# Kernel tuning notes

Hardware: AMD Instinct MI355X
Metric: run time of the kernel (lower is better)

Reference implementation:

```python
import jax, jax.numpy as jnp
import numpy as np

D_MODEL, D_K, D_V = 1024, 64, 128
NUM_HEAD = D_MODEL // D_V  # 8


def setup_inputs() -> dict:
    key = jax.random.key(0)
    ks = jax.random.split(key, 6)
    B, SQ, SKV = 4, 2048, 2048
    return {
        "encoder_output": jax.random.normal(ks[0], (B, SKV, D_MODEL), jnp.float32),
        "pre_output": jax.random.normal(ks[1], (B, SQ, D_MODEL), jnp.float32),
        "Wq": jax.random.normal(ks[2], (D_MODEL, D_K * NUM_HEAD), jnp.float32) * 0.02,
        "Wk": jax.random.normal(ks[3], (D_MODEL, D_K * NUM_HEAD), jnp.float32) * 0.02,
        "Wv": jax.random.normal(ks[4], (D_MODEL, D_MODEL), jnp.float32) * 0.02,
        "Wo": jax.random.normal(ks[5], (D_MODEL, D_MODEL), jnp.float32) * 0.02,
    }


def reference(encoder_output, pre_output, Wq, Wk, Wv, Wo):
    B, SQ, _ = pre_output.shape
    SKV = encoder_output.shape[1]
    # projections (Linear, bias=False)
    q = pre_output @ Wq          # [B, SQ, H*d_k]
    k = encoder_output @ Wk      # [B, SKV, H*d_k]
    v = encoder_output @ Wv      # [B, SKV, H*d_v] (= d_model)
    # per-head contiguous slices == reshape into head dim
    q = q.reshape(B, SQ, NUM_HEAD, D_K)
    k = k.reshape(B, SKV, NUM_HEAD, D_K)
    v = v.reshape(B, SKV, NUM_HEAD, D_V)
    scale = 1.0 / np.sqrt(D_K).astype(np.float32)
    scores = jnp.einsum("bqhd,bkhd->bhqk", q, k) * scale  # [B,H,SQ,SKV]
    attn = jax.nn.softmax(scores, axis=-1)
    out = jnp.einsum("bhqk,bkhd->bqhd", attn, v)           # [B,SQ,H,d_v]
    out = out.reshape(B, SQ, NUM_HEAD * D_V)               # concat heads
    return out @ Wo
```

## Files before the change

### kernel.cpp

```cpp
#include <hip/hip_runtime.h>
#include <math.h>

#define D_MODEL 1024
#define DK 64
#define DV 128
#define NH 8
#define BB 4
#define SQL 2048
#define SKV 2048

typedef __bf16 bf16x8 __attribute__((ext_vector_type(8)));
typedef float f32x4 __attribute__((ext_vector_type(4)));

#if __has_builtin(__builtin_amdgcn_exp2f)
#define EXP2(x) __builtin_amdgcn_exp2f(x)
#else
#define EXP2(x) exp2f(x)
#endif

#define MFMA16(a, b, c) __builtin_amdgcn_mfma_f32_16x16x32_bf16(a, b, c, 0, 0, 0)

__device__ __forceinline__ ushort f2bf(float f) {
  unsigned u = __float_as_uint(f);
  u += 0x7FFFu + ((u >> 16) & 1u);
  return (ushort)(u >> 16);
}
__device__ __forceinline__ unsigned pk2bf(float lo, float hi) {
  unsigned ul = __float_as_uint(lo);
  unsigned uh = __float_as_uint(hi);
  ul += 0x7FFFu + ((ul >> 16) & 1u);
  uh += 0x7FFFu + ((uh >> 16) & 1u);
  return __builtin_amdgcn_perm(uh, ul, 0x07060302u);
}

#define GLDS16(g, l)                                                       \
  __builtin_amdgcn_global_load_lds(                                        \
      (const __attribute__((address_space(1))) unsigned int*)(g),          \
      (__attribute__((address_space(3))) unsigned int*)(l), 16, 0, 0)

__global__ __launch_bounds__(256) void cvt2_kernel(
    const float* __restrict__ s0, const float* __restrict__ s1,
    ushort* __restrict__ d0, ushort* __restrict__ d1, int n4) {
  const float* src = blockIdx.z ? s1 : s0;
  ushort* dst = blockIdx.z ? d1 : d0;
  int i = blockIdx.x * 256 + threadIdx.x;
  if (i >= n4) return;
  float4 v = ((const float4*)src)[i];
  ushort4 o;
  o.x = f2bf(v.x); o.y = f2bf(v.y); o.z = f2bf(v.z); o.w = f2bf(v.w);
  ((ushort4*)dst)[i] = o;
}

__global__ __launch_bounds__(256) void cvt_t4_kernel(
    const float* __restrict__ W0, const float* __restrict__ W1,
    const float* __restrict__ W2, const float* __restrict__ W3,
    ushort* __restrict__ T0, ushort* __restrict__ T1, ushort* __restrict__ T2,
    ushort* __restrict__ T3) {
  __shared__ ushort T[32][34];
  const int z = blockIdx.z;
  const int C = (z < 2) ? 512 : 1024;
  const int c0 = blockIdx.y * 32;
  if (c0 >= C) return;
  const float* W = (z == 0) ? W0 : (z == 1) ? W1 : (z == 2) ? W2 : W3;
  ushort* Wt = (z == 0) ? T0 : (z == 1) ? T1 : (z == 2) ? T2 : T3;
  const int R = 1024;
  const int r0 = blockIdx.x * 32;
  const int tx = threadIdx.x, ty = threadIdx.y;
#pragma unroll
  for (int i = 0; i < 4; ++i) {
    const int rr = ty + i * 8;
    T[rr][tx] = f2bf(W[(size_t)(r0 + rr) * C + c0 + tx]);
  }
  __syncthreads();
#pragma unroll
  for (int i = 0; i < 4; ++i) {
    const int rr = ty + i * 8;
    Wt[(size_t)(c0 + rr) * R + r0 + tx] = T[tx][rr];
  }
}

__device__ __forceinline__ void gemm_core_acc(ushort* sh, const ushort* At,
                                              const ushort* Bt, int K,
                                              f32x4 (&acc)[4][4]) {
  const int t = threadIdx.x;
  const int w = t >> 6, lane = t & 63;
  const int wm = (w >> 1) * 64, wn = (w & 1) * 64;
  const int lr = lane & 15, quad = lane >> 4;

  const int r0 = t >> 2;
  const int lb = (t & 3) ^ ((r0 >> 1) & 3);
  const ushort* gA0 = At + (size_t)r0 * K + lb * 8;
  const ushort* gA1 = At + (size_t)(r0 + 64) * K + lb * 8;
  const ushort* gB0 = Bt + (size_t)r0 * K + lb * 8;
  const ushort* gB1 = Bt + (size_t)(r0 + 64) * K + lb * 8;

  const int sw = (quad ^ ((lr >> 1) & 3)) * 8;

#pragma unroll
  for (int i = 0; i < 4; ++i)
#pragma unroll
    for (int j = 0; j < 4; ++j) acc[i][j] = (f32x4){0.f, 0.f, 0.f, 0.f};

  auto stage = [&](int k0, int buf) {
    ushort* d = sh + buf * 8192 + t * 8;
    GLDS16(gA0 + k0, d);
    GLDS16(gA1 + k0, d + 2048);
    GLDS16(gB0 + k0, d + 4096);
    GLDS16(gB1 + k0, d + 6144);
  };

  const int NT = K >> 5;
  stage(0, 0);
  for (int ti = 0; ti < NT; ++ti) {
    const bool more = (ti + 1 < NT);
    if (more) {
      stage((ti + 1) * 32, (ti + 1) & 1);
      asm volatile("s_waitcnt vmcnt(4)" ::: "memory");
    } else {
      asm volatile("s_waitcnt vmcnt(0)" ::: "memory");
    }
    __builtin_amdgcn_s_barrier();
    __builtin_amdgcn_sched_barrier(0);
    const ushort(*A)[32] = (const ushort(*)[32])(sh + (ti & 1) * 8192);
    const ushort(*B)[32] = (const ushort(*)[32])(sh + (ti & 1) * 8192 + 4096);
    bf16x8 fa[4], fb[4];
#pragma unroll
    for (int i = 0; i < 4; ++i) fa[i] = *(const bf16x8*)&A[wm + i * 16 + lr][sw];
#pragma unroll
    for (int j = 0; j < 4; ++j) fb[j] = *(const bf16x8*)&B[wn + j * 16 + lr][sw];
#pragma unroll
    for (int i = 0; i < 4; ++i)
#pragma unroll
      for (int j = 0; j < 4; ++j) acc[i][j] = MFMA16(fa[i], fb[j], acc[i][j]);
    __builtin_amdgcn_sched_barrier(0);
    if (more) __builtin_amdgcn_s_barrier();
  }
}

__global__ __launch_bounds__(256) void gemm_qkv_kernel(
    const ushort* __restrict__ preb, const ushort* __restrict__ encb,
    const ushort* __restrict__ WqkvT, ushort* __restrict__ qb,
    ushort* __restrict__ kb, ushort* __restrict__ vt, float qsc) {
  __shared__ __attribute__((aligned(16))) ushort shm[17408];

  const int nlin = blockIdx.x + 16 * blockIdx.y;
  const int l = (nlin & 7) * 128 + (nlin >> 3);
  const int n0 = (l & 15) * 128, m0 = (l >> 4) * 128;

  const int t = threadIdx.x;
  const int w = t >> 6, lane = t & 63;
  const int wm = (w >> 1) * 64, wn = (w & 1) * 64;
  const int lr = lane & 15, quad = lane >> 4;

  const ushort* A = (n0 < 512) ? preb : encb;
  f32x4 acc[4][4];
  gemm_core_acc(shm, A + (size_t)m0 * D_MODEL, WqkvT + (size_t)n0 * D_MODEL,
                D_MODEL, acc);

  if (n0 < 1024) {
    ushort* C = (n0 < 512) ? qb : kb;
    const int ncol = (n0 < 512) ? n0 : n0 - 512;
    const float osc = (n0 < 512) ? qsc : 1.f;
#pragma unroll
    for (int i = 0; i < 4; ++i)
#pragma unroll
      for (int j = 0; j < 4; ++j)
#pragma unroll
        for (int r = 0; r < 4; ++r) {
          const int row = m0 + wm + i * 16 + quad * 4 + r;
          const int col = ncol + wn + j * 16 + lr;
          C[(size_t)row * 512 + col] = f2bf(acc[i][j][r] * osc);
        }
  } else {
    const int h = (n0 - 1024) >> 7;
    const int b = m0 >> 11;
    const int skv0 = m0 & 2047;
    __syncthreads();
    ushort(*Ep)[68] = (ushort(*)[68])(shm + w * 4352);
#pragma unroll
    for (int i = 0; i < 4; ++i)
#pragma unroll
      for (int j = 0; j < 4; ++j) {
        uint2 dd;
        dd.x = pk2bf(acc[i][j][0], acc[i][j][1]);
        dd.y = pk2bf(acc[i][j][2], acc[i][j][3]);
        *(uint2*)&Ep[j * 16 + lr][i * 16 + quad * 4] = dd;
      }
    ushort* vbase =
        vt + ((size_t)(b * NH + h) * DV + wn) * SKV + skv0 + wm;
#pragma unroll
    for (int rep = 0; rep < 8; ++rep) {
      const int dvl = (lane >> 3) + rep * 8;
      const int skvc = (lane & 7) * 8;
      *(uint4*)&vbase[(size_t)dvl * SKV + skvc] = *(const uint4*)&Ep[dvl][skvc];
    }
  }
}

__global__ __launch_bounds__(256) void gemm_o_kernel(
    const ushort* __restrict__ ao, const ushort* __restrict__ WoT,
    float* __restrict__ out) {
  __shared__ __attribute__((aligned(16))) ushort sh[16384];
  const int nlin = blockIdx.x + 8 * blockIdx.y;
  const int l = (nlin & 7) * 64 + (nlin >> 3);
  const int n0 = (l & 7) * 128, m0 = (l >> 3) * 128;
  const int t = threadIdx.x;
  const int w = t >> 6, lane = t & 63;
  const int wm = (w >> 1) * 64, wn = (w & 1) * 64;
  const int lr = lane & 15, quad = lane >> 4;
  f32x4 acc[4][4];
  gemm_core_acc(sh, ao + (size_t)m0 * D_MODEL, WoT + (size_t)n0 * D_MODEL,
                D_MODEL, acc);
#pragma unroll
  for (int i = 0; i < 4; ++i)
#pragma unroll
    for (int j = 0; j < 4; ++j)
#pragma unroll
      for (int r = 0; r < 4; ++r) {
        const int row = m0 + wm + i * 16 + quad * 4 + r;
        const int col = n0 + wn + j * 16 + lr;
        out[(size_t)row * D_MODEL + col] = acc[i][j][r];
      }
}

__global__ __launch_bounds__(256) void attn_mfma_kernel(
    const ushort* __restrict__ Q, const ushort* __restrict__ Kb,
    const ushort* __restrict__ Vt, ushort* __restrict__ Oo) {
  __shared__ ushort Ks[2][64][64];
  __shared__ ushort Vs[2][128][64];
  __shared__ ushort Ps[4][32][36];

  const int t = threadIdx.x;
  const int n = blockIdx.x + 16 * blockIdx.y + 128 * blockIdx.z;
  const int l = (n & 7) * 64 + (n >> 3);
  const int qt = l & 15, h = (l >> 4) & 7, b = l >> 7;

  const int w = t >> 6, lane = t & 63;
  const int lr = lane & 15, quad = lane >> 4;
  const int q0 = qt * 128 + w * 32;
  const int swk = lr & 7;

  union { bf16x8 v; ushort u[8]; } one8;
#pragma unroll
  for (int i = 0; i < 8; ++i) one8.u[i] = 0x3F80;

  bf16x8 aq[2][2];
#pragma unroll
  for (int mt = 0; mt < 2; ++mt)
#pragma unroll
    for (int kh = 0; kh < 2; ++kh)
      aq[mt][kh] = *(const bf16x8*)&Q[(size_t)(b * SQL + q0 + mt * 16 + lr) *
                                          (NH * DK) +
                                      h * DK + kh * 32 + quad * 8];

  f32x4 accO[2][9];
#pragma unroll
  for (int mt = 0; mt < 2; ++mt)
#pragma unroll
    for (int dn = 0; dn < 9; ++dn) accO[mt][dn] = (f32x4){0.f, 0.f, 0.f, 0.f};

  const ushort* kbase = Kb + (size_t)b * SKV * (NH * DK) + h * DK;
  const ushort* vbase = Vt + (size_t)(b * NH + h) * DV * SKV;

  const int srow = t >> 3;
  const int sb7 = (t & 7) ^ (srow & 7);
  const ushort* gK = kbase + (size_t)srow * (NH * DK) + sb7 * 8;
  const ushort* gV = vbase + (size_t)srow * SKV + sb7 * 8;
  ushort* dK = (ushort*)Ks + t * 8;
  ushort* dV = (ushort*)Vs + t * 8;

  auto stage = [&](int kv0, int buf) {
    const ushort* gk = gK + (size_t)kv0 * (NH * DK);
    ushort* dk = dK + buf * 4096;
    GLDS16(gk, dk);
    GLDS16(gk + (size_t)32 * (NH * DK), dk + 2048);
    const ushort* gv = gV + kv0;
    ushort* dv = dV + buf * 8192;
    GLDS16(gv, dv);
    GLDS16(gv + (size_t)32 * SKV, dv + 2048);
    GLDS16(gv + (size_t)64 * SKV, dv + 4096);
    GLDS16(gv + (size_t)96 * SKV, dv + 6144);
  };

  auto sexp = [&](const ushort(*Kc)[64], int c, bf16x8 (&ap)[2]) {
#pragma unroll
    for (int tt = 0; tt < 2; ++tt) {
      const int nt = c * 2 + tt;
      const bf16x8 fk0 = *(const bf16x8*)&Kc[nt * 16 + lr][(quad ^ swk) * 8];
      const bf16x8 fk1 =
          *(const bf16x8*)&Kc[nt * 16 + lr][((4 + quad) ^ swk) * 8];
#pragma unroll
      for (int mt = 0; mt < 2; ++mt) {
        f32x4 s = (f32x4){0.f, 0.f, 0.f, 0.f};
        s = MFMA16(fk0, aq[mt][0], s);
        s = MFMA16(fk1, aq[mt][1], s);
        const unsigned u0 = __float_as_uint(EXP2(s[0]));
        const unsigned u1 = __float_as_uint(EXP2(s[1]));
        const unsigned u2 = __float_as_uint(EXP2(s[2]));
        const unsigned u3 = __float_as_uint(EXP2(s[3]));
        uint2 dd;
        dd.x = __builtin_amdgcn_perm(u1, u0, 0x07060302u);
        dd.y = __builtin_amdgcn_perm(u3, u2, 0x07060302u);
        *(uint2*)&Ps[w][mt * 16 + lr][tt * 16 + quad * 4] = dd;
      }
    }
#pragma unroll
    for (int mt = 0; mt < 2; ++mt) {
      union { bf16x8 v; uint2 u[2]; } fr;
      fr.u[0] = *(const uint2*)&Ps[w][mt * 16 + lr][quad * 8];
      fr.u[1] = *(const uint2*)&Ps[w][mt * 16 + lr][quad * 8 + 4];
      ap[mt] = fr.v;
    }
  };

  auto pv = [&](const bf16x8 (&ap)[2], const ushort(*Vc)[64], int c) {
#pragma unroll
    for (int dn = 0; dn < 8; ++dn) {
      const bf16x8 fv =
          *(const bf16x8*)&Vc[dn * 16 + lr][((c * 4 + quad) ^ swk) * 8];
      accO[0][dn] = MFMA16(ap[0], fv, accO[0][dn]);
      accO[1][dn] = MFMA16(ap[1], fv, accO[1][dn]);
    }
    accO[0][8] = MFMA16(ap[0], one8.v, accO[0][8]);
    accO[1][8] = MFMA16(ap[1], one8.v, accO[1][8]);
  };

  stage(0, 0);
  for (int ti = 0; ti < 31; ++ti) {
    stage((ti + 1) * 64, (ti + 1) & 1);
    asm volatile("s_waitcnt vmcnt(6)" ::: "memory");
    __builtin_amdgcn_s_barrier();
    __builtin_amdgcn_sched_barrier(0);
    const ushort(*Kc)[64] = Ks[ti & 1];
    const ushort(*Vc)[64] = Vs[ti & 1];
    __builtin_amdgcn_s_setprio(1);
    bf16x8 apA[2], apB[2];
    sexp(Kc, 0, apA);
    sexp(Kc, 1, apB);
    pv(apA, Vc, 0);
    pv(apB, Vc, 1);
    __builtin_amdgcn_s_setprio(0);
    __builtin_amdgcn_sched_barrier(0);
    __builtin_amdgcn_s_barrier();
  }
  asm volatile("s_waitcnt vmcnt(0)" ::: "memory");
  __builtin_amdgcn_s_barrier();
  __builtin_amdgcn_sched_barrier(0);
  {
    __builtin_amdgcn_s_setprio(1);
    bf16x8 apA[2], apB[2];
    sexp(Ks[1], 0, apA);
    sexp(Ks[1], 1, apB);
    pv(apA, Vs[1], 0);
    pv(apB, Vs[1], 1);
    __builtin_amdgcn_s_setprio(0);
  }

#pragma unroll
  for (int mt = 0; mt < 2; ++mt) {
    float inv[4];
#pragma unroll
    for (int r = 0; r < 4; ++r) inv[r] = 1.f / accO[mt][8][r];
#pragma unroll
    for (int dn = 0; dn < 8; ++dn)
#pragma unroll
      for (int r = 0; r < 4; ++r) {
        const size_t row = (size_t)b * SQL + q0 + mt * 16 + quad * 4 + r;
        Oo[row * D_MODEL + h * DV + dn * 16 + lr] =
            f2bf(accO[mt][dn][r] * inv[r]);
      }
  }
}

extern "C" void kernel_launch(void* const* d_in, const int* in_sizes, int n_in,
                              void* d_out, int out_size, void* d_ws,
                              size_t ws_size, hipStream_t stream) {
  const float* enc = (const float*)d_in[0];
  const float* pre = (const float*)d_in[1];
  const float* Wq = (const float*)d_in[2];
  const float* Wk = (const float*)d_in[3];
  const float* Wv = (const float*)d_in[4];
  const float* Wo = (const float*)d_in[5];
  float* out = (float*)d_out;

  const int M = BB * SQL;

  ushort* encb = (ushort*)d_ws;
  ushort* preb = encb + (size_t)M * D_MODEL;
  ushort* WqT = preb + (size_t)M * D_MODEL;
  ushort* WkT = WqT + (size_t)(NH * DK) * D_MODEL;
  ushort* WvT = WkT + (size_t)(NH * DK) * D_MODEL;
  ushort* WoT = WvT + (size_t)D_MODEL * D_MODEL;
  ushort* qb = WoT + (size_t)D_MODEL * D_MODEL;
  ushort* kb = qb + (size_t)M * (NH * DK);
  ushort* vt = kb + (size_t)M * (NH * DK);
  ushort* ao = encb;

  const int n4 = M * D_MODEL / 4;
  dim3 blk(256);
  dim3 tblk(32, 8);

  cvt2_kernel<<<dim3(n4 / 256, 1, 2), blk, 0, stream>>>(enc, pre, encb, preb,
                                                        n4);
  cvt_t4_kernel<<<dim3(32, 32, 4), tblk, 0, stream>>>(Wq, Wk, Wv, Wo, WqT, WkT,
                                                      WvT, WoT);

  gemm_qkv_kernel<<<dim3(16, 64), blk, 0, stream>>>(
      preb, encb, WqT, qb, kb, vt, 0.18033688011112042f);

  attn_mfma_kernel<<<dim3(SQL / 128, NH, BB), blk, 0, stream>>>(qb, kb, vt, ao);

  gemm_o_kernel<<<dim3(8, 64), blk, 0, stream>>>(ao, WoT, out);
}
```

Before: 256.1 us.

## Split attention block into 8 waves of 16 query rows each

Raises the attention kernel from 256 to 512 threads, with each wave handling 16 query rows instead of 32, so per-wave accumulators and Q fragments are halved. K/V staging is spread over more threads, so each thread issues fewer global-to-LDS loads and the wait count is adjusted to match. The aim is more waves in flight for latency hiding and lower register pressure. In exchange, every wave must read each K/V fragment from LDS for half as many rows, which doubles LDS read traffic per MFMA, and barriers now synchronise more waves.

```diff
diff --git a/kernel.cpp b/kernel.cpp
--- a/kernel.cpp
+++ b/kernel.cpp
@@ -223,12 +223,12 @@
       }
 }
 
-__global__ __launch_bounds__(256) void attn_mfma_kernel(
+__global__ __launch_bounds__(512) void attn_mfma_kernel(
     const ushort* __restrict__ Q, const ushort* __restrict__ Kb,
     const ushort* __restrict__ Vt, ushort* __restrict__ Oo) {
   __shared__ ushort Ks[2][64][64];
   __shared__ ushort Vs[2][128][64];
-  __shared__ ushort Ps[4][32][36];
+  __shared__ ushort Ps[8][16][36];
 
   const int t = threadIdx.x;
   const int n = blockIdx.x + 16 * blockIdx.y + 128 * blockIdx.z;
@@ -237,27 +237,22 @@
 
   const int w = t >> 6, lane = t & 63;
   const int lr = lane & 15, quad = lane >> 4;
-  const int q0 = qt * 128 + w * 32;
+  const int q0 = qt * 128 + w * 16;
   const int swk = lr & 7;
 
   union { bf16x8 v; ushort u[8]; } one8;
 #pragma unroll
   for (int i = 0; i < 8; ++i) one8.u[i] = 0x3F80;
 
-  bf16x8 aq[2][2];
-#pragma unroll
-  for (int mt = 0; mt < 2; ++mt)
-#pragma unroll
-    for (int kh = 0; kh < 2; ++kh)
-      aq[mt][kh] = *(const bf16x8*)&Q[(size_t)(b * SQL + q0 + mt * 16 + lr) *
-                                          (NH * DK) +
-                                      h * DK + kh * 32 + quad * 8];
-
-  f32x4 accO[2][9];
-#pragma unroll
-  for (int mt = 0; mt < 2; ++mt)
-#pragma unroll
-    for (int dn = 0; dn < 9; ++dn) accO[mt][dn] = (f32x4){0.f, 0.f, 0.f, 0.f};
+  bf16x8 aq[2];
+#pragma unroll
+  for (int kh = 0; kh < 2; ++kh)
+    aq[kh] = *(const bf16x8*)&Q[(size_t)(b * SQL + q0 + lr) * (NH * DK) +
+                                h * DK + kh * 32 + quad * 8];
+
+  f32x4 accO[9];
+#pragma unroll
+  for (int dn = 0; dn < 9; ++dn) accO[dn] = (f32x4){0.f, 0.f, 0.f, 0.f};
 
   const ushort* kbase = Kb + (size_t)b * SKV * (NH * DK) + h * DK;
   const ushort* vbase = Vt + (size_t)(b * NH + h) * DV * SKV;
@@ -270,71 +265,58 @@
   ushort* dV = (ushort*)Vs + t * 8;
 
   auto stage = [&](int kv0, int buf) {
-    const ushort* gk = gK + (size_t)kv0 * (NH * DK);
-    ushort* dk = dK + buf * 4096;
-    GLDS16(gk, dk);
-    GLDS16(gk + (size_t)32 * (NH * DK), dk + 2048);
+    GLDS16(gK + (size_t)kv0 * (NH * DK), dK + buf * 4096);
     const ushort* gv = gV + kv0;
     ushort* dv = dV + buf * 8192;
     GLDS16(gv, dv);
-    GLDS16(gv + (size_t)32 * SKV, dv + 2048);
     GLDS16(gv + (size_t)64 * SKV, dv + 4096);
-    GLDS16(gv + (size_t)96 * SKV, dv + 6144);
   };
 
-  auto sexp = [&](const ushort(*Kc)[64], int c, bf16x8 (&ap)[2]) {
+  auto sexp = [&](const ushort(*Kc)[64], int c, bf16x8& ap) {
 #pragma unroll
     for (int tt = 0; tt < 2; ++tt) {
       const int nt = c * 2 + tt;
       const bf16x8 fk0 = *(const bf16x8*)&Kc[nt * 16 + lr][(quad ^ swk) * 8];
       const bf16x8 fk1 =
           *(const bf16x8*)&Kc[nt * 16 + lr][((4 + quad) ^ swk) * 8];
-#pragma unroll
-      for (int mt = 0; mt < 2; ++mt) {
-        f32x4 s = (f32x4){0.f, 0.f, 0.f, 0.f};
-        s = MFMA16(fk0, aq[mt][0], s);
-        s = MFMA16(fk1, aq[mt][1], s);
-        const unsigned u0 = __float_as_uint(EXP2(s[0]));
-        const unsigned u1 = __float_as_uint(EXP2(s[1]));
-        const unsigned u2 = __float_as_uint(EXP2(s[2]));
-        const unsigned u3 = __float_as_uint(EXP2(s[3]));
-        uint2 dd;
-        dd.x = __builtin_amdgcn_perm(u1, u0, 0x07060302u);
-        dd.y = __builtin_amdgcn_perm(u3, u2, 0x07060302u);
-        *(uint2*)&Ps[w][mt * 16 + lr][tt * 16 + quad * 4] = dd;
-      }
+      f32x4 s = (f32x4){0.f, 0.f, 0.f, 0.f};
+      s = MFMA16(fk0, aq[0], s);
+      s = MFMA16(fk1, aq[1], s);
+      const unsigned u0 = __float_as_uint(EXP2(s[0]));
+      const unsigned u1 = __float_as_uint(EXP2(s[1]));
+      const unsigned u2 = __float_as_uint(EXP2(s[2]));
+      const unsigned u3 = __float_as_uint(EXP2(s[3]));
+      uint2 dd;
+      dd.x = __builtin_amdgcn_perm(u1, u0, 0x07060302u);
+      dd.y = __builtin_amdgcn_perm(u3, u2, 0x07060302u);
+      *(uint2*)&Ps[w][lr][tt * 16 + quad * 4] = dd;
     }
-#pragma unroll
-    for (int mt = 0; mt < 2; ++mt) {
-      union { bf16x8 v; uint2 u[2]; } fr;
-      fr.u[0] = *(const uint2*)&Ps[w][mt * 16 + lr][quad * 8];
-      fr.u[1] = *(const uint2*)&Ps[w][mt * 16 + lr][quad * 8 + 4];
-      ap[mt] = fr.v;
-    }
+    union { bf16x8 v; uint2 u[2]; } fr;
+    fr.u[0] = *(const uint2*)&Ps[w][lr][quad * 8];
+    fr.u[1] = *(const uint2*)&Ps[w][lr][quad * 8 + 4];
+    ap = fr.v;
   };
 
-  auto pv = [&](const bf16x8 (&ap)[2], const ushort(*Vc)[64], int c) {
+  auto pv = [&](const bf16x8& ap, const ushort(*Vc)[64], int c) {
 #pragma unroll
     for (int dn = 0; dn < 8; ++dn) {
       const bf16x8 fv =
           *(const bf16x8*)&Vc[dn * 16 + lr][((c * 4 + quad) ^ swk) * 8];
-      accO[0][dn] = MFMA16(ap[0], fv, accO[0][dn]);
-      accO[1][dn] = MFMA16(ap[1], fv, accO[1][dn]);
+      accO[dn] = MFMA16(ap, fv, accO[dn]);
     }
-    accO[0][8] = MFMA16(ap[0], one8.v, accO[0][8]);
-    accO[1][8] = MFMA16(ap[1], one8.v, accO[1][8]);
+    accO[8] = MFMA16(ap, one8.v, accO[8]);
   };
 
   stage(0, 0);
   for (int ti = 0; ti < 31; ++ti) {
     stage((ti + 1) * 64, (ti + 1) & 1);
-    asm volatile("s_waitcnt vmcnt(6)" ::: "memory");
+    asm volatile("s_waitcnt vmcnt(3)" ::: "memory");
     __builtin_amdgcn_s_barrier();
     __builtin_amdgcn_sched_barrier(0);
     const ushort(*Kc)[64] = Ks[ti & 1];
     const ushort(*Vc)[64] = Vs[ti & 1];
     __builtin_amdgcn_s_setprio(1);
-    bf16x8 apA[2], apB[2];
+    bf16x8 apA, apB;
     sexp(Kc, 0, apA);
     sexp(Kc, 1, apB);
     pv(apA, Vc, 0);
@@ -348,7 +330,7 @@
   __builtin_amdgcn_sched_barrier(0);
   {
     __builtin_amdgcn_s_setprio(1);
-    bf16x8 apA[2], apB[2];
+    bf16x8 apA, apB;
     sexp(Ks[1], 0, apA);
     sexp(Ks[1], 1, apB);
     pv(apA, Vs[1], 0);
@@ -356,18 +338,17 @@
     __builtin_amdgcn_s_setprio(0);
   }
 
-#pragma unroll
-  for (int mt = 0; mt < 2; ++mt) {
+  {
     float inv[4];
 #pragma unroll
-    for (int r = 0; r < 4; ++r) inv[r] = 1.f / accO[mt][8][r];
+    for (int r = 0; r < 4; ++r) inv[r] = 1.f / accO[8][r];
 #pragma unroll
     for (int dn = 0; dn < 8; ++dn)
 #pragma unroll
       for (int r = 0; r < 4; ++r) {
-        const size_t row = (size_t)b * SQL + q0 + mt * 16 + quad * 4 + r;
+        const size_t row = (size_t)b * SQL + q0 + quad * 4 + r;
         Oo[row * D_MODEL + h * DV + dn * 16 + lr] =
-            f2bf(accO[mt][dn][r] * inv[r]);
+            f2bf(accO[dn][r] * inv[r]);
       }
   }
 }
@@ -408,7 +389,8 @@
   gemm_qkv_kernel<<<dim3(16, 64), blk, 0, stream>>>(
       preb, encb, WqT, qb, kb, vt, 0.18033688011112042f);
 
-  attn_mfma_kernel<<<dim3(SQL / 128, NH, BB), blk, 0, stream>>>(qb, kb, vt, ao);
+  attn_mfma_kernel<<<dim3(SQL / 128, NH, BB), dim3(512), 0, stream>>>(qb, kb,
+                                                                      vt, ao);
 
   gemm_o_kernel<<<dim3(8, 64), blk, 0, stream>>>(ao, WoT, out);
 }
```

Measured after the change: 256.5 us. Within noise of the previous version (+0.2%).
